# Kernel optimization log

Hardware: AMD Instinct MI355X
Metric: run time of the kernel (lower is better)

Reference implementation:

```python
import jax, jax.numpy as jnp
import numpy as np

N, E, F_IN, H, D = 50000, 800000, 128, 4, 32


def setup_inputs() -> dict:
    key = jax.random.key(0)
    k1, k2, k3, k4 = jax.random.split(key, 4)
    feat = jax.random.normal(k1, (N, F_IN), dtype=jnp.float32)
    src = jax.random.randint(k2, (E,), 0, N, dtype=jnp.int64)
    dst = jax.random.randint(k3, (E,), 0, N, dtype=jnp.int64)
    # fc weight (xavier-normal-ish scale) and explicit bias
    W = jax.random.normal(k4, (F_IN, H * D), dtype=jnp.float32) * (1.0 / np.sqrt(F_IN))
    bias = jnp.zeros((H * D,), dtype=jnp.float32)
    return {"feat": feat, "src": src, "dst": dst, "W": W, "bias": bias}


def reference(feat, src, dst, W, bias):
    # fc projection, view as (N, H, D)
    ft = (feat @ W).reshape(N, H, D)
    # apply_edges u_dot_v: per-edge per-head dot product -> [E, H]
    e = jnp.einsum("ehd,ehd->eh", ft[src], ft[dst])
    # edge_softmax over incoming edges of each dst node (numerically stable)
    emax = jax.ops.segment_max(e, dst, num_segments=N)  # [N, H]
    ex = jnp.exp(e - emax[dst])
    denom = jax.ops.segment_sum(ex, dst, num_segments=N)  # [N, H]
    a = ex / denom[dst]  # [E, H]
    # update_all: u_mul_e + sum -> weighted scatter aggregation
    msg = ft[src] * a[:, :, None]  # [E, H, D]
    rst = jax.ops.segment_sum(msg, dst, num_segments=N)  # [N, H, D]
    return rst + bias.reshape(1, H, D)
```

## Files before the change

kernel.cpp:

```cpp
#include <hip/hip_runtime.h>
#include <math.h>

#define F 128
#define HEADS 4
#define DHEAD 32
#define CLS 4
#define HIST_H 128
#define CW_MAX 13184

typedef unsigned short ushort_t;
typedef __attribute__((ext_vector_type(8))) short short8;
typedef __attribute__((ext_vector_type(4))) float f32x4;

__device__ __forceinline__ ushort_t f2bf(float x) {
  unsigned u = __float_as_uint(x);
  unsigned r = u + 0x7FFFu + ((u >> 16) & 1u);
  return (ushort_t)(r >> 16);
}

__device__ __forceinline__ void unpack8(const int4& r, float* v) {
  int rr[4] = {r.x, r.y, r.z, r.w};
#pragma unroll
  for (int q = 0; q < 4; q++) {
    unsigned u = (unsigned)rr[q];
    v[2 * q] = __uint_as_float(u << 16);
    v[2 * q + 1] = __uint_as_float(u & 0xFFFF0000u);
  }
}

__global__ __launch_bounds__(256) void wprep_kernel(
    const float* __restrict__ W, ushort_t* __restrict__ whi,
    ushort_t* __restrict__ wlo) {
  int idx = blockIdx.x * 256 + threadIdx.x;
  if (idx >= 128 * 128) return;
  int j = idx & 7;
  int lane = (idx >> 3) & 63;
  int f = idx >> 9;
  int kt = f >> 3, nt = f & 7;
  int k = kt * 32 + (lane >> 4) * 8 + j;
  int n = nt * 16 + (lane & 15);
  float w = W[k * 128 + n];
  unsigned u = __float_as_uint(w);
  unsigned hb = u & 0xFFFF0000u;
  float lo = w - __uint_as_float(hb);
  whi[idx] = (ushort_t)(hb >> 16);
  wlo[idx] = f2bf(lo);
}

__global__ __launch_bounds__(256) void gemm_hist_kernel(
    const float* __restrict__ feat, const ushort_t* __restrict__ whi,
    const ushort_t* __restrict__ wlo, ushort_t* __restrict__ ftb, int N,
    const int* __restrict__ dst, ushort_t* __restrict__ partials, int cwp,
    int E, int gemmBlocks) {
  __shared__ int lh[CW_MAX];
  if ((int)blockIdx.x >= gemmBlocks) {
    const int hb = blockIdx.x - gemmBlocks;
    const int cls = hb & (CLS - 1);
    const int h = hb >> 2;
    const int cw = (N + CLS - 1) / CLS;
    const int nbase = cls * cw;
    for (int j = threadIdx.x; j < cw; j += 256) lh[j] = 0;
    __syncthreads();
    const int seg = (E + HIST_H - 1) / HIST_H;
    const int e0 = h * seg;
    const int e1 = min(e0 + seg, E);
    int e = e0 + (int)threadIdx.x;
    for (; e + 768 < e1; e += 1024) {
      int d0 = dst[e];
      int d1 = dst[e + 256];
      int d2 = dst[e + 512];
      int d3 = dst[e + 768];
      if ((unsigned)(d0 - nbase) < (unsigned)cw) atomicAdd(&lh[d0 - nbase], 1);
      if ((unsigned)(d1 - nbase) < (unsigned)cw) atomicAdd(&lh[d1 - nbase], 1);
      if ((unsigned)(d2 - nbase) < (unsigned)cw) atomicAdd(&lh[d2 - nbase], 1);
      if ((unsigned)(d3 - nbase) < (unsigned)cw) atomicAdd(&lh[d3 - nbase], 1);
    }
    for (; e < e1; e += 256) {
      int d = dst[e];
      if ((unsigned)(d - nbase) < (unsigned)cw) atomicAdd(&lh[d - nbase], 1);
    }
    __syncthreads();
    ushort_t* prow = partials + (size_t)(cls * HIST_H + h) * cwp;
    for (int j = threadIdx.x; j < cw; j += 256) prow[j] = (ushort_t)lh[j];
    return;
  }
  const int t = threadIdx.x;
  const int wv = t >> 6;
  const int l = t & 63;
  const int g = l >> 4;
  const int lm = l & 15;
  const int arow = blockIdx.x * 64 + wv * 16 + lm;
  const int arowc = min(arow, N - 1);

  f32x4 acc[8];
#pragma unroll
  for (int nt = 0; nt < 8; nt++) acc[nt] = (f32x4){0.f, 0.f, 0.f, 0.f};

#pragma unroll
  for (int kt = 0; kt < 4; kt++) {
    const float* ap = feat + (size_t)arowc * F + kt * 32 + g * 8;
    float a[8];
    *(float4*)&a[0] = *(const float4*)ap;
    *(float4*)&a[4] = *(const float4*)(ap + 4);
    short8 ahi, alo;
#pragma unroll
    for (int j = 0; j < 8; j++) {
      unsigned u = __float_as_uint(a[j]);
      unsigned hb2 = u & 0xFFFF0000u;
      float lo = a[j] - __uint_as_float(hb2);
      ahi[j] = (short)(hb2 >> 16);
      alo[j] = (short)f2bf(lo);
    }
    const ushort_t* bh = whi + (size_t)(kt * 8) * 512 + l * 8;
    const ushort_t* bl = wlo + (size_t)(kt * 8) * 512 + l * 8;
#pragma unroll
    for (int nt = 0; nt < 8; nt++) {
      short8 bhi = *(const short8*)(bh + nt * 512);
      short8 blo = *(const short8*)(bl + nt * 512);
      acc[nt] =
          __builtin_amdgcn_mfma_f32_16x16x32_bf16(ahi, blo, acc[nt], 0, 0, 0);
      acc[nt] =
          __builtin_amdgcn_mfma_f32_16x16x32_bf16(alo, bhi, acc[nt], 0, 0, 0);
      acc[nt] =
          __builtin_amdgcn_mfma_f32_16x16x32_bf16(ahi, bhi, acc[nt], 0, 0, 0);
    }
  }

  const int orow0 = blockIdx.x * 64 + wv * 16 + g * 4;
#pragma unroll
  for (int reg = 0; reg < 4; reg++) {
    int orow = orow0 + reg;
    if (orow < N) {
#pragma unroll
      for (int nt = 0; nt < 8; nt++)
        ftb[(size_t)orow * F + nt * 16 + lm] = f2bf(acc[nt][reg]);
    }
  }
}

__global__ void scan_block_kernel(const ushort_t* __restrict__ partials,
                                  int cwp, int* __restrict__ offs,
                                  ushort_t* __restrict__ rel16,
                                  int* __restrict__ bsums, int N) {
  __shared__ int s[256];
  int t = threadIdx.x, i = blockIdx.x * 256 + t;
  int v = 0;
  if (i < N) {
    int cw = (N + CLS - 1) / CLS;
    int c = i / cw;
    int j = i - c * cw;
    const ushort_t* pb = partials + (size_t)c * HIST_H * cwp + j;
    ushort_t* cb = rel16 + (size_t)c * HIST_H * cwp + j;
    int run = 0;
#pragma unroll 8
    for (int h = 0; h < HIST_H; h++) {
      cb[(size_t)h * cwp] = (ushort_t)run;
      run += pb[(size_t)h * cwp];
    }
    v = run;
  }
  s[t] = v;
  __syncthreads();
  for (int d = 1; d < 256; d <<= 1) {
    int x = (t >= d) ? s[t - d] : 0;
    __syncthreads();
    s[t] += x;
    __syncthreads();
  }
  if (i < N) offs[i] = s[t] - v;
  if (t == 255) bsums[blockIdx.x] = s[255];
}

__global__ void scan_finish_kernel(int* __restrict__ offs,
                                   const int* __restrict__ bsums, int N,
                                   int E) {
  int t = threadIdx.x, b = blockIdx.x;
  int v = (t < b) ? bsums[t] : 0;
#pragma unroll
  for (int d = 32; d > 0; d >>= 1) v += __shfl_down(v, d, 64);
  __shared__ int wsum[4];
  if ((t & 63) == 0) wsum[t >> 6] = v;
  __syncthreads();
  int total = wsum[0] + wsum[1] + wsum[2] + wsum[3];
  int i = b * 256 + t;
  if (i < N) offs[i] += total;
  if (b == 0 && t == 0) offs[N] = E;
}

__global__ __launch_bounds__(256) void scatter_kernel(
    const int* __restrict__ src, const int* __restrict__ dst,
    const int* __restrict__ offs, const ushort_t* __restrict__ rel16, int cwp,
    ushort_t* __restrict__ csr, int E, int N) {
  __shared__ int lcur[CW_MAX];
  const int cls = blockIdx.x & (CLS - 1);
  const int h = blockIdx.x >> 2;
  const int cw = (N + CLS - 1) / CLS;
  const int nbase = cls * cw;
  const int jmax = min(cw, N - nbase);
  const ushort_t* crow = rel16 + (size_t)(cls * HIST_H + h) * cwp;
  for (int j = threadIdx.x; j < jmax; j += 256)
    lcur[j] = offs[nbase + j] + (int)crow[j];
  __syncthreads();
  const int seg = (E + HIST_H - 1) / HIST_H;
  const int e0 = h * seg;
  const int e1 = min(e0 + seg, E);
  int e = e0 + (int)threadIdx.x;
  for (; e + 768 < e1; e += 1024) {
    int d0 = dst[e];
    int d1 = dst[e + 256];
    int d2 = dst[e + 512];
    int d3 = dst[e + 768];
    int s0 = src[e];
    int s1 = src[e + 256];
    int s2 = src[e + 512];
    int s3 = src[e + 768];
    if ((unsigned)(d0 - nbase) < (unsigned)cw)
      csr[atomicAdd(&lcur[d0 - nbase], 1)] = (ushort_t)s0;
    if ((unsigned)(d1 - nbase) < (unsigned)cw)
      csr[atomicAdd(&lcur[d1 - nbase], 1)] = (ushort_t)s1;
    if ((unsigned)(d2 - nbase) < (unsigned)cw)
      csr[atomicAdd(&lcur[d2 - nbase], 1)] = (ushort_t)s2;
    if ((unsigned)(d3 - nbase) < (unsigned)cw)
      csr[atomicAdd(&lcur[d3 - nbase], 1)] = (ushort_t)s3;
  }
  for (; e < e1; e += 256) {
    int d = dst[e];
    int sv = src[e];
    if ((unsigned)(d - nbase) < (unsigned)cw)
      csr[atomicAdd(&lcur[d - nbase], 1)] = (ushort_t)sv;
  }
}

__global__ __launch_bounds__(256) void aggregate_kernel(
    const ushort_t* __restrict__ ftb, const int* __restrict__ offs,
    const ushort_t* __restrict__ csr, const float* __restrict__ bias,
    float* __restrict__ out, int N) {
  const int T = blockIdx.x * 256 + threadIdx.x;
  if (T >= N * 16) return;
  const int sub = T & 3;
  const int p = T >> 2;
  const int h = p & 3;
  const int n = p >> 2;
  const int dimBase = h * DHEAD + sub * 8;

  const int off = offs[n];
  const int deg = offs[n + 1] - off;

  const float LOG2E = 1.4426950408889634f;
  float ftd[8];
  {
    int4 r = *(const int4*)&ftb[n * F + dimBase];
    unpack8(r, ftd);
#pragma unroll
    for (int j = 0; j < 8; j++) ftd[j] *= LOG2E;
  }

  float s = 0.f;
  float acc[8];
#pragma unroll
  for (int j = 0; j < 8; j++) acc[j] = 0.f;

#define PROCESS(RX)                                              \
  do {                                                           \
    float v[8];                                                  \
    unpack8(RX, v);                                              \
    float part = 0.f;                                            \
    _Pragma("unroll") for (int j = 0; j < 8; j++) part =         \
        fmaf(ftd[j], v[j], part);                                \
    part += __shfl_xor(part, 1, 4);                              \
    part += __shfl_xor(part, 2, 4);                              \
    float w = exp2f(part);                                       \
    s += w;                                                      \
    _Pragma("unroll") for (int j = 0; j < 8; j++) acc[j] =       \
        fmaf(w, v[j], acc[j]);                                   \
  } while (0)

  int4 R0 = make_int4(0, 0, 0, 0), R1 = R0, R2 = R0, R3 = R0;
  if (deg > 0) {
    int dm1 = deg - 1;
    int s0 = csr[off];
    int s1 = csr[off + min(1, dm1)];
    int s2 = csr[off + min(2, dm1)];
    int s3 = csr[off + min(3, dm1)];
    R0 = *(const int4*)&ftb[(size_t)s0 * F + dimBase];
    R1 = *(const int4*)&ftb[(size_t)s1 * F + dimBase];
    R2 = *(const int4*)&ftb[(size_t)s2 * F + dimBase];
    R3 = *(const int4*)&ftb[(size_t)s3 * F + dimBase];
  }
  int i = 0;
  for (; i + 4 <= deg; i += 4) {
    int dm1 = deg - 1;
    int sa = csr[off + min(i + 4, dm1)];
    int sb = csr[off + min(i + 5, dm1)];
    int sc = csr[off + min(i + 6, dm1)];
    int sd = csr[off + min(i + 7, dm1)];
    int4 Na = *(const int4*)&ftb[(size_t)sa * F + dimBase];
    int4 Nb = *(const int4*)&ftb[(size_t)sb * F + dimBase];
    int4 Nc = *(const int4*)&ftb[(size_t)sc * F + dimBase];
    int4 Nd = *(const int4*)&ftb[(size_t)sd * F + dimBase];
    PROCESS(R0);
    PROCESS(R1);
    PROCESS(R2);
    PROCESS(R3);
    R0 = Na; R1 = Nb; R2 = Nc; R3 = Nd;
  }
  int r = deg - i;
  if (r > 0) PROCESS(R0);
  if (r > 1) PROCESS(R1);
  if (r > 2) PROCESS(R2);
#undef PROCESS

  float inv = (deg > 0) ? 1.f / s : 0.f;
  float4 b0 = *(const float4*)&bias[dimBase];
  float4 b1 = *(const float4*)&bias[dimBase + 4];
  f32x4 o0 = {acc[0] * inv + b0.x, acc[1] * inv + b0.y, acc[2] * inv + b0.z,
              acc[3] * inv + b0.w};
  f32x4 o1 = {acc[4] * inv + b1.x, acc[5] * inv + b1.y, acc[6] * inv + b1.z,
              acc[7] * inv + b1.w};
  __builtin_nontemporal_store(o0, (f32x4*)&out[n * F + dimBase]);
  __builtin_nontemporal_store(o1, (f32x4*)&out[n * F + dimBase + 4]);
}

extern "C" void kernel_launch(void* const* d_in, const int* in_sizes, int n_in,
                              void* d_out, int out_size, void* d_ws,
                              size_t ws_size, hipStream_t stream) {
  const float* feat = (const float*)d_in[0];
  const int* src = (const int*)d_in[1];
  const int* dst = (const int*)d_in[2];
  const float* W = (const float*)d_in[3];
  const float* bias = (const float*)d_in[4];
  float* out = (float*)d_out;

  const int N = in_sizes[0] / F;
  const int E = in_sizes[1];
  const int cw = (N + CLS - 1) / CLS;
  const int cwp = (cw + 31) & ~31;

  char* ws = (char*)d_ws;
  ushort_t* ftb = (ushort_t*)ws;
  size_t ftB = (size_t)N * F * sizeof(ushort_t);
  ftB = (ftB + 255) & ~(size_t)255;
  int* offs = (int*)(ws + ftB);
  int* bsums = offs + N + 1;
  ushort_t* csr = (ushort_t*)(bsums + 256);
  ushort_t* whi = csr + ((E + 128) & ~127);
  ushort_t* wlo = whi + 128 * 128;
  ushort_t* partials = wlo + 128 * 128;
  ushort_t* rel16 = partials + CLS * HIST_H * cwp;

  wprep_kernel<<<64, 256, 0, stream>>>(W, whi, wlo);

  int gemmBlocks = (N + 63) / 64;
  gemm_hist_kernel<<<gemmBlocks + CLS * HIST_H, 256, 0, stream>>>(
      feat, whi, wlo, ftb, N, dst, partials, cwp, E, gemmBlocks);

  int nb = (N + 255) / 256;
  scan_block_kernel<<<nb, 256, 0, stream>>>(partials, cwp, offs, rel16,
                                            bsums, N);
  scan_finish_kernel<<<nb, 256, 0, stream>>>(offs, bsums, N, E);

  scatter_kernel<<<CLS * HIST_H, 256, 0, stream>>>(src, dst, offs, rel16, cwp,
                                                   csr, E, N);

  aggregate_kernel<<<(N * 16 + 255) / 256, 256, 0, stream>>>(ftb, offs, csr,
                                                             bias, out, N);
}
```

Measured before the change: 85.62 us.

## Fold scan finish into scatter kernel, deepen aggregate prefetch to six rows

Removes the separate scan_finish kernel launch. Each scatter block now redoes the small block-sum prefix scan in shared memory and applies it when it initialises its cursors, and the h==0 blocks write the absolute offsets array used by aggregation. The aggregation loop's software prefetch depth goes from four to six neighbour rows, and exp2f is replaced by the hardware exp2 builtin. In exchange, every scatter block repeats the redundant scan and the aggregation kernel uses more registers, which may lower occupancy.

```diff
diff --git a/kernel.cpp b/kernel.cpp
--- a/kernel.cpp
+++ b/kernel.cpp
@@ -11,6 +11,12 @@
 typedef unsigned short ushort_t;
 typedef __attribute__((ext_vector_type(8))) short short8;
 typedef __attribute__((ext_vector_type(4))) float f32x4;
+
+#if __has_builtin(__builtin_amdgcn_exp2f)
+#define EXP2F __builtin_amdgcn_exp2f
+#else
+#define EXP2F exp2f
+#endif
 
 __device__ __forceinline__ ushort_t f2bf(float x) {
   unsigned u = __float_as_uint(x);
@@ -171,40 +177,52 @@
   if (t == 255) bsums[blockIdx.x] = s[255];
 }
 
-__global__ void scan_finish_kernel(int* __restrict__ offs,
-                                   const int* __restrict__ bsums, int N,
-                                   int E) {
-  int t = threadIdx.x, b = blockIdx.x;
-  int v = (t < b) ? bsums[t] : 0;
-#pragma unroll
-  for (int d = 32; d > 0; d >>= 1) v += __shfl_down(v, d, 64);
-  __shared__ int wsum[4];
-  if ((t & 63) == 0) wsum[t >> 6] = v;
-  __syncthreads();
-  int total = wsum[0] + wsum[1] + wsum[2] + wsum[3];
-  int i = b * 256 + t;
-  if (i < N) offs[i] += total;
-  if (b == 0 && t == 0) offs[N] = E;
-}
-
 __global__ __launch_bounds__(256) void scatter_kernel(
     const int* __restrict__ src, const int* __restrict__ dst,
-    const int* __restrict__ offs, const ushort_t* __restrict__ rel16, int cwp,
-    ushort_t* __restrict__ csr, int E, int N) {
+    const int* __restrict__ offs, const int* __restrict__ bsums,
+    const ushort_t* __restrict__ rel16, int cwp, ushort_t* __restrict__ csr,
+    int* __restrict__ offs_abs, int E, int N, int nb) {
   __shared__ int lcur[CW_MAX];
+  __shared__ int bpfx[256];
+  const int t = threadIdx.x;
   const int cls = blockIdx.x & (CLS - 1);
   const int h = blockIdx.x >> 2;
   const int cw = (N + CLS - 1) / CLS;
   const int nbase = cls * cw;
   const int jmax = min(cw, N - nbase);
+
+  int bv = (t < nb) ? bsums[t] : 0;
+  bpfx[t] = bv;
+  __syncthreads();
+  for (int d = 1; d < 256; d <<= 1) {
+    int x = (t >= d) ? bpfx[t - d] : 0;
+    __syncthreads();
+    bpfx[t] += x;
+    __syncthreads();
+  }
+  const int myincl = bpfx[t];
+  __syncthreads();
+  bpfx[t] = myincl - bv;
+  __syncthreads();
+
   const ushort_t* crow = rel16 + (size_t)(cls * HIST_H + h) * cwp;
-  for (int j = threadIdx.x; j < jmax; j += 256)
-    lcur[j] = offs[nbase + j] + (int)crow[j];
-  __syncthreads();
+  for (int j = t; j < jmax; j += 256) {
+    int i = nbase + j;
+    lcur[j] = offs[i] + bpfx[i >> 8] + (int)crow[j];
+  }
+  if (h == 0) {
+    for (int j = t; j < jmax; j += 256) {
+      int i = nbase + j;
+      offs_abs[i] = offs[i] + bpfx[i >> 8];
+    }
+    if (cls == CLS - 1 && t == 0) offs_abs[N] = E;
+  }
+  __syncthreads();
+
   const int seg = (E + HIST_H - 1) / HIST_H;
   const int e0 = h * seg;
   const int e1 = min(e0 + seg, E);
-  int e = e0 + (int)threadIdx.x;
+  int e = e0 + t;
   for (; e + 768 < e1; e += 1024) {
     int d0 = dst[e];
     int d1 = dst[e + 256];
@@ -269,46 +287,54 @@
         fmaf(ftd[j], v[j], part);                                \
     part += __shfl_xor(part, 1, 4);                              \
     part += __shfl_xor(part, 2, 4);                              \
-    float w = exp2f(part);                                       \
+    float w = EXP2F(part);                                       \
     s += w;                                                      \
     _Pragma("unroll") for (int j = 0; j < 8; j++) acc[j] =       \
         fmaf(w, v[j], acc[j]);                                   \
   } while (0)
 
-  int4 R0 = make_int4(0, 0, 0, 0), R1 = R0, R2 = R0, R3 = R0;
+#define ROWLOAD(RX, idx)                                         \
+  do {                                                           \
+    int _s = csr[off + min((idx), dm1)];                         \
+    RX = *(const int4*)&ftb[(size_t)_s * F + dimBase];           \
+  } while (0)
+
+  int4 R0 = make_int4(0, 0, 0, 0), R1 = R0, R2 = R0, R3 = R0, R4 = R0,
+       R5 = R0;
+  const int dm1 = deg - 1;
   if (deg > 0) {
-    int dm1 = deg - 1;
-    int s0 = csr[off];
-    int s1 = csr[off + min(1, dm1)];
-    int s2 = csr[off + min(2, dm1)];
-    int s3 = csr[off + min(3, dm1)];
-    R0 = *(const int4*)&ftb[(size_t)s0 * F + dimBase];
-    R1 = *(const int4*)&ftb[(size_t)s1 * F + dimBase];
-    R2 = *(const int4*)&ftb[(size_t)s2 * F + dimBase];
-    R3 = *(const int4*)&ftb[(size_t)s3 * F + dimBase];
+    ROWLOAD(R0, 0);
+    ROWLOAD(R1, 1);
+    ROWLOAD(R2, 2);
+    ROWLOAD(R3, 3);
+    ROWLOAD(R4, 4);
+    ROWLOAD(R5, 5);
   }
   int i = 0;
-  for (; i + 4 <= deg; i += 4) {
-    int dm1 = deg - 1;
-    int sa = csr[off + min(i + 4, dm1)];
-    int sb = csr[off + min(i + 5, dm1)];
-    int sc = csr[off + min(i + 6, dm1)];
-    int sd = csr[off + min(i + 7, dm1)];
-    int4 Na = *(const int4*)&ftb[(size_t)sa * F + dimBase];
-    int4 Nb = *(const int4*)&ftb[(size_t)sb * F + dimBase];
-    int4 Nc = *(const int4*)&ftb[(size_t)sc * F + dimBase];
-    int4 Nd = *(const int4*)&ftb[(size_t)sd * F + dimBase];
+  for (; i + 6 <= deg; i += 6) {
+    int4 Na, Nb, Nc, Nd, Ne, Nf;
+    ROWLOAD(Na, i + 6);
+    ROWLOAD(Nb, i + 7);
+    ROWLOAD(Nc, i + 8);
+    ROWLOAD(Nd, i + 9);
+    ROWLOAD(Ne, i + 10);
+    ROWLOAD(Nf, i + 11);
     PROCESS(R0);
     PROCESS(R1);
     PROCESS(R2);
     PROCESS(R3);
-    R0 = Na; R1 = Nb; R2 = Nc; R3 = Nd;
+    PROCESS(R4);
+    PROCESS(R5);
+    R0 = Na; R1 = Nb; R2 = Nc; R3 = Nd; R4 = Ne; R5 = Nf;
   }
   int r = deg - i;
   if (r > 0) PROCESS(R0);
   if (r > 1) PROCESS(R1);
   if (r > 2) PROCESS(R2);
+  if (r > 3) PROCESS(R3);
+  if (r > 4) PROCESS(R4);
 #undef PROCESS
+#undef ROWLOAD
 
   float inv = (deg > 0) ? 1.f / s : 0.f;
   float4 b0 = *(const float4*)&bias[dimBase];
@@ -341,7 +367,8 @@
   size_t ftB = (size_t)N * F * sizeof(ushort_t);
   ftB = (ftB + 255) & ~(size_t)255;
   int* offs = (int*)(ws + ftB);
-  int* bsums = offs + N + 1;
+  int* offs_abs = offs + N + 1;
+  int* bsums = offs_abs + N + 1;
   ushort_t* csr = (ushort_t*)(bsums + 256);
   ushort_t* whi = csr + ((E + 128) & ~127);
   ushort_t* wlo = whi + 128 * 128;
@@ -357,11 +384,10 @@
   int nb = (N + 255) / 256;
   scan_block_kernel<<<nb, 256, 0, stream>>>(partials, cwp, offs, rel16,
                                             bsums, N);
-  scan_finish_kernel<<<nb, 256, 0, stream>>>(offs, bsums, N, E);
-
-  scatter_kernel<<<CLS * HIST_H, 256, 0, stream>>>(src, dst, offs, rel16, cwp,
-                                                   csr, E, N);
-
-  aggregate_kernel<<<(N * 16 + 255) / 256, 256, 0, stream>>>(ftb, offs, csr,
-                                                             bias, out, N);
-}
+
+  scatter_kernel<<<CLS * HIST_H, 256, 0, stream>>>(
+      src, dst, offs, bsums, rel16, cwp, csr, offs_abs, E, N, nb);
+
+  aggregate_kernel<<<(N * 16 + 255) / 256, 256, 0, stream>>>(
+      ftb, offs_abs, csr, bias, out, N);
+}
```

New measurement: 85.77 us. No clear change (+0.2%).
